# Kernel optimization log

Measured on AMD Instinct MI355X. Metric: run time of the kernel, lower is better.

The kernel has to match this reference:

```python
import jax, jax.numpy as jnp
import numpy as np

H = W = 512
P = H * W          # total superpixel member pixels
N_SP = 1024        # number of superpixels


def _conv(x, w, b):
    # x: [N,C,H,W], w: [O,I,3,3] -> [N,O,H,W], SAME padding
    y = jax.lax.conv_general_dilated(
        x, w, window_strides=(1, 1), padding='SAME',
        dimension_numbers=('NCHW', 'OIHW', 'NCHW'))
    return y + b[None, :, None, None]


def _embed(raw, w1, b1, w2, b2, w3, b3):
    h = jax.nn.relu(_conv(raw, w1, b1))
    h = jax.nn.relu(_conv(h, w2, b2))
    return _conv(h, w3, b3)  # [1, 10, H, W]


def setup_inputs() -> dict:
    key = jax.random.key(0)
    ks = jax.random.split(key, 6)
    raw = jax.random.normal(ks[0], (1, 1, H, W), dtype=jnp.float32)
    w1 = jax.random.normal(ks[1], (64, 1, 3, 3), dtype=jnp.float32) * 0.3
    b1 = jnp.zeros((64,), jnp.float32)
    w2 = jax.random.normal(ks[2], (64, 64, 3, 3), dtype=jnp.float32) * 0.05
    b2 = jnp.zeros((64,), jnp.float32)
    w3 = jax.random.normal(ks[3], (10, 64, 3, 3), dtype=jnp.float32) * 0.05
    b3 = jnp.zeros((10,), jnp.float32)
    pix_rc = jax.random.randint(ks[4], (P, 2), 0, H, dtype=jnp.int32)
    seg_ids = jax.random.randint(ks[5], (P,), 0, N_SP, dtype=jnp.int32)
    return {"raw": raw, "w1": w1, "b1": b1, "w2": w2, "b2": b2,
            "w3": w3, "b3": b3, "pix_rc": pix_rc, "seg_ids": seg_ids,
            "n_sp": N_SP}


def reference(raw, w1, b1, w2, b2, w3, b3, pix_rc, seg_ids, n_sp):
    feats = _embed(raw, w1, b1, w2, b2, w3, b3)  # [1, C, H, W]
    f = feats[0]                                  # [C, H, W]
    # gather per-pixel feature vectors: [P, C]
    vals = f[:, pix_rc[:, 0], pix_rc[:, 1]].T
    # scatter-mean over superpixels (= per-sp sum / mass)
    sums = jax.ops.segment_sum(vals, seg_ids, num_segments=n_sp)      # [n_sp, C]
    cnts = jax.ops.segment_sum(jnp.ones((vals.shape[0],), vals.dtype),
                               seg_ids, num_segments=n_sp)            # [n_sp]
    return sums / jnp.maximum(cnts, 1.0)[:, None]
```

## Files before the change

### kernel.cpp

```cpp
#include <hip/hip_runtime.h>

typedef __attribute__((ext_vector_type(8))) short short8;
typedef __attribute__((ext_vector_type(4))) float f32x4;

constexpr int H = 512, W = 512;
constexpr int P = H * W;
constexpr int NSP = 1024;
constexpr int SBLK = 512;
constexpr int FGRP = 16;

__device__ inline unsigned short f2bf(float f) {
  unsigned u = __builtin_bit_cast(unsigned, f);
  unsigned r = (u + 0x7fffu + ((u >> 16) & 1u)) >> 16;
  return (unsigned short)r;
}
__device__ inline float bflo(unsigned u) { return __builtin_bit_cast(float, u << 16); }
__device__ inline float bfhi(unsigned u) { return __builtin_bit_cast(float, u & 0xffff0000u); }

__device__ inline int xcd_swz(int b, int cpx) { return (b & 7) * cpx + (b >> 3); }

__global__ __launch_bounds__(256) void prep_k(const float* __restrict__ w2,
                                              const float* __restrict__ w3,
                                              unsigned short* __restrict__ wt2s,
                                              unsigned short* __restrict__ wt3s,
                                              unsigned short* __restrict__ zeros) {
  if (blockIdx.x == 0 && threadIdx.x < 128) zeros[threadIdx.x] = 0;
  int i = blockIdx.x * 256 + threadIdx.x;
  if (i < 36864) {
    int k = i >> 11;
    int t = (i >> 3) & 255;
    int e = i & 7;
    int r = t >> 2, sp = t & 3, s = sp ^ (r & 3);
    int tap = k >> 1, ic = (k & 1) * 32 + s * 8 + e;
    wt2s[i] = f2bf(w2[r * 576 + ic * 9 + tap]);
  } else if (i < 46080) {
    int j = i - 36864;
    int k = j >> 9;
    int t = (j >> 3) & 63;
    int e = j & 7;
    int r = t >> 2, sp = t & 3, s = sp ^ (r & 3);
    int tap = k >> 1, ic = (k & 1) * 32 + s * 8 + e;
    wt3s[j] = (r < 10) ? f2bf(w3[r * 576 + ic * 9 + tap]) : (unsigned short)0;
  }
}

__device__ inline void stage_acts(const unsigned short* __restrict__ xin,
                                  const unsigned short* __restrict__ zeros,
                                  unsigned short* acts, int r0, int c0,
                                  int wave, int lane) {
  for (int wi = wave; wi < 26; wi += 4) {
    int cidx = wi * 64 + lane;
    int pix = cidx >> 3, slotp = cidx & 7;
    int prow = pix / 34, pcol = pix - prow * 34;
    int gr = r0 + prow - 1, gc = c0 + pcol - 1;
    int slot = slotp ^ (pix & 7);
    bool ok = (pix < 204) & ((unsigned)gr < 512u) & ((unsigned)gc < 512u);
    const unsigned short* src = ok ? (xin + (((size_t)(gr * 512 + gc)) << 6) + slot * 8) : zeros;
    unsigned short* dstb = &acts[wi * 512];
    __builtin_amdgcn_global_load_lds((const __attribute__((address_space(1))) void*)src,
                                     (__attribute__((address_space(3))) void*)dstb, 16, 0, 0);
  }
}

__global__ __launch_bounds__(256) void conv2_k(const float* __restrict__ raw,
                                               const float* __restrict__ w1,
                                               const float* __restrict__ b1,
                                               const unsigned short* __restrict__ wts,
                                               const float* __restrict__ bias,
                                               unsigned short* __restrict__ ynhwc) {
  constexpr int WCS = 2048;
  __shared__ __align__(16) unsigned short acts[208 * 64];
  __shared__ __align__(16) unsigned short wbuf[3 * WCS];
  __shared__ float rawt[9 * 36];
  int tid = threadIdx.x;
  int lane = tid & 63, wave = tid >> 6;
  int logical = xcd_swz(blockIdx.x, 256);
  int tilex = logical & 15, tiley = logical >> 4;
  int c0 = tilex * 32, r0 = tiley * 4;

#pragma unroll
  for (int k0 = 0; k0 < 2; ++k0) {
    const unsigned short* src = wts + (size_t)k0 * WCS + tid * 8;
    unsigned short* dstb = wbuf + k0 * WCS + wave * 512;
    __builtin_amdgcn_global_load_lds((const __attribute__((address_space(1))) void*)src,
                                     (__attribute__((address_space(3))) void*)dstb, 16, 0, 0);
  }
  for (int i = tid; i < 324; i += 256) {
    int rr = i / 36, cc = i - rr * 36;
    int gr = r0 + rr - 2, gc = c0 + cc - 2;
    bool ok = ((unsigned)gr < 512u) && ((unsigned)gc < 512u);
    rawt[i] = ok ? raw[gr * 512 + gc] : 0.f;
  }

  int q = lane >> 4, n = lane & 15;
  short8 a1f;
  {
    short av[8];
#pragma unroll
    for (int e = 0; e < 8; ++e) av[e] = 0;
    int oc = wave * 16 + n;
    if (q == 0) {
#pragma unroll
      for (int e = 0; e < 8; ++e) av[e] = (short)f2bf(w1[oc * 9 + e]);
    } else if (q == 1) {
      av[0] = (short)f2bf(w1[oc * 9 + 8]);
    }
    a1f = (short8){av[0], av[1], av[2], av[3], av[4], av[5], av[6], av[7]};
  }
  float bb1[4];
#pragma unroll
  for (int r2 = 0; r2 < 4; ++r2) bb1[r2] = b1[wave * 16 + q * 4 + r2];
  __syncthreads();

  char* actw = (char*)acts;
  for (int t = 0; t < 13; ++t) {
    int px = t * 16 + n;
    int prow = px / 34, pcol = px - prow * 34;
    short bv[8];
#pragma unroll
    for (int e = 0; e < 8; ++e) bv[e] = 0;
    if (q == 0) {
#pragma unroll
      for (int e = 0; e < 8; ++e) {
        int dy = e / 3, dx = e - dy * 3;
        bv[e] = (short)f2bf(rawt[(prow + dy) * 36 + pcol + dx]);
      }
    } else if (q == 1) {
      bv[0] = (short)f2bf(rawt[(prow + 2) * 36 + pcol + 2]);
    }
    short8 b1f = (short8){bv[0], bv[1], bv[2], bv[3], bv[4], bv[5], bv[6], bv[7]};
    f32x4 d = __builtin_amdgcn_mfma_f32_16x16x32_bf16(a1f, b1f,
                                                       (f32x4){0.f, 0.f, 0.f, 0.f}, 0, 0, 0);
    int gr1 = r0 + prow - 1, gc1 = c0 + pcol - 1;
    bool ok1 = ((unsigned)gr1 < 512u) && ((unsigned)gc1 < 512u);
    float o0 = ok1 ? fmaxf(d.x + bb1[0], 0.f) : 0.f;
    float o1 = ok1 ? fmaxf(d.y + bb1[1], 0.f) : 0.f;
    float o2 = ok1 ? fmaxf(d.z + bb1[2], 0.f) : 0.f;
    float o3 = ok1 ? fmaxf(d.w + bb1[3], 0.f) : 0.f;
    unsigned lo = (unsigned)f2bf(o0) | ((unsigned)f2bf(o1) << 16);
    unsigned hi = (unsigned)f2bf(o2) | ((unsigned)f2bf(o3) << 16);
    int wa = px * 128 + ((((wave * 2 + (q >> 1)) ^ (px & 7)) << 4)) + ((q & 1) << 3);
    *reinterpret_cast<uint2*>(actw + wa) = make_uint2(lo, hi);
  }
  __syncthreads();

  f32x4 acc[4][2];
#pragma unroll
  for (int og = 0; og < 4; ++og)
#pragma unroll
    for (int g = 0; g < 2; ++g) acc[og][g] = (f32x4){0.f, 0.f, 0.f, 0.f};

  int plbase[2];
#pragma unroll
  for (int g = 0; g < 2; ++g) plbase[g] = wave * 34 + 16 * g + n;
  const char* actb = (const char*)acts;

#pragma unroll
  for (int k = 0; k < 18; ++k) {
    if (k == 17) {
      asm volatile("s_waitcnt vmcnt(0)" ::: "memory");
    } else {
      asm volatile("s_waitcnt vmcnt(1)" ::: "memory");
    }
    __builtin_amdgcn_sched_barrier(0);
    __builtin_amdgcn_s_barrier();
    __builtin_amdgcn_sched_barrier(0);
    if (k + 2 < 18) {
      const unsigned short* src = wts + (size_t)(k + 2) * WCS + tid * 8;
      unsigned short* dstb = wbuf + ((k + 2) % 3) * WCS + wave * 512;
      __builtin_amdgcn_global_load_lds((const __attribute__((address_space(1))) void*)src,
                                       (__attribute__((address_space(3))) void*)dstb, 16, 0, 0);
    }
    const int tap = k >> 1, kc = k & 1;
    const int kyy = tap / 3, kxx = tap - kyy * 3;
    const char* wb = (const char*)(wbuf + (k % 3) * WCS);
    short8 af[4];
#pragma unroll
    for (int og = 0; og < 4; ++og) {
      int r = og * 16 + n;
      af[og] = *reinterpret_cast<const short8*>(wb + r * 64 + ((q ^ (r & 3)) * 16));
    }
#pragma unroll
    for (int g = 0; g < 2; ++g) {
      int pl = plbase[g] + kyy * 34 + kxx;
      int addr = pl * 128 + (((kc * 4 + q) ^ (pl & 7)) * 16);
      short8 bf = *reinterpret_cast<const short8*>(actb + addr);
#pragma unroll
      for (int og = 0; og < 4; ++og)
        acc[og][g] = __builtin_amdgcn_mfma_f32_16x16x32_bf16(af[og], bf, acc[og][g], 0, 0, 0);
    }
  }

  __syncthreads();
  char* ob = (char*)acts;
#pragma unroll
  for (int og = 0; og < 4; ++og) {
    float b0 = bias[og * 16 + q * 4 + 0], b1v = bias[og * 16 + q * 4 + 1];
    float b2 = bias[og * 16 + q * 4 + 2], b3 = bias[og * 16 + q * 4 + 3];
#pragma unroll
    for (int g = 0; g < 2; ++g) {
      int pl = wave * 32 + g * 16 + n;
      f32x4 v = acc[og][g];
      float o0 = fmaxf(v.x + b0, 0.f), o1 = fmaxf(v.y + b1v, 0.f);
      float o2 = fmaxf(v.z + b2, 0.f), o3 = fmaxf(v.w + b3, 0.f);
      unsigned lo = (unsigned)f2bf(o0) | ((unsigned)f2bf(o1) << 16);
      unsigned hi = (unsigned)f2bf(o2) | ((unsigned)f2bf(o3) << 16);
      int lslot = og * 2 + (q >> 1);
      int wa = pl * 128 + (((lslot ^ (pl & 7)) << 4)) + ((q & 1) << 3);
      *reinterpret_cast<uint2*>(ob + wa) = make_uint2(lo, hi);
    }
  }
  __syncthreads();
  char* yb = (char*)ynhwc;
#pragma unroll
  for (int it = 0; it < 4; ++it) {
    int c = it * 256 + tid;
    int pl = c >> 3, slot = c & 7;
    uint4 v = *reinterpret_cast<const uint4*>(ob + pl * 128 + ((slot ^ (pl & 7)) << 4));
    size_t gb = (((size_t)(r0 + (pl >> 5)) * 512) + c0 + (pl & 31)) * 128 + slot * 16;
    *reinterpret_cast<uint4*>(yb + gb) = v;
  }
}

__global__ __launch_bounds__(256) void conv3_k(const unsigned short* __restrict__ xin,
                                               const unsigned short* __restrict__ wts,
                                               const float* __restrict__ bias,
                                               unsigned short* __restrict__ feats,
                                               const unsigned short* __restrict__ zeros) {
  __shared__ __align__(16) unsigned short acts[208 * 64];
  __shared__ __align__(16) unsigned short wl[9216];
  int tid = threadIdx.x;
  int lane = tid & 63, wave = tid >> 6;
  int logical = xcd_swz(blockIdx.x, 256);
  int tilex = logical & 15, tiley = logical >> 4;
  int c0 = tilex * 32, r0 = tiley * 4;

  stage_acts(xin, zeros, acts, r0, c0, wave, lane);
  for (int wi = wave; wi < 18; wi += 4) {
    const unsigned short* src = wts + (size_t)wi * 512 + lane * 8;
    unsigned short* dstb = &wl[wi * 512];
    __builtin_amdgcn_global_load_lds((const __attribute__((address_space(1))) void*)src,
                                     (__attribute__((address_space(3))) void*)dstb, 16, 0, 0);
  }
  __syncthreads();

  int q = lane >> 4, n = lane & 15;
  f32x4 acc[2];
#pragma unroll
  for (int g = 0; g < 2; ++g) acc[g] = (f32x4){0.f, 0.f, 0.f, 0.f};
  int plbase[2];
#pragma unroll
  for (int g = 0; g < 2; ++g) plbase[g] = wave * 34 + 16 * g + n;
  const char* actb = (const char*)acts;
  const char* wb0 = (const char*)wl;

#pragma unroll
  for (int k = 0; k < 18; ++k) {
    const int tap = k >> 1, kc = k & 1;
    const int kyy = tap / 3, kxx = tap - kyy * 3;
    short8 af = *reinterpret_cast<const short8*>(wb0 + k * 1024 + n * 64 + ((q ^ (n & 3)) * 16));
#pragma unroll
    for (int g = 0; g < 2; ++g) {
      int pl = plbase[g] + kyy * 34 + kxx;
      int addr = pl * 128 + (((kc * 4 + q) ^ (pl & 7)) * 16);
      short8 bf = *reinterpret_cast<const short8*>(actb + addr);
      acc[g] = __builtin_amdgcn_mfma_f32_16x16x32_bf16(af, bf, acc[g], 0, 0, 0);
    }
  }

  __syncthreads();
  char* ob = (char*)acts;
  float bb[4];
#pragma unroll
  for (int r2 = 0; r2 < 4; ++r2) {
    int oc = q * 4 + r2;
    bb[r2] = (oc < 10) ? bias[oc] : 0.f;
  }
#pragma unroll
  for (int g = 0; g < 2; ++g) {
    int pl = wave * 32 + g * 16 + n;
    f32x4 v = acc[g];
    float o0 = v.x + bb[0], o1 = v.y + bb[1], o2 = v.z + bb[2], o3 = v.w + bb[3];
    if (q < 2) {
      unsigned u0 = (unsigned)f2bf(o0) | ((unsigned)f2bf(o1) << 16);
      unsigned u1 = (unsigned)f2bf(o2) | ((unsigned)f2bf(o3) << 16);
      *reinterpret_cast<uint2*>(ob + pl * 24 + q * 8) = make_uint2(u0, u1);
    } else if (q == 2) {
      *reinterpret_cast<unsigned*>(ob + pl * 24 + 16) =
          (unsigned)f2bf(o0) | ((unsigned)f2bf(o1) << 16);
    }
  }
  __syncthreads();
  char* fb = (char*)feats;
  {
    int c = tid;
    for (int it = 0; it < 3 && c < 640; ++it, c += 256) {
      int row = c / 160, wb = c - row * 160;
      int byte = wb * 4;
      int px = byte / 20, off = byte - px * 20;
      unsigned v = *reinterpret_cast<const unsigned*>(ob + (row * 32 + px) * 24 + off);
      size_t gbyte = (((size_t)(r0 + row) * 512) + c0) * 20 + (size_t)byte;
      *reinterpret_cast<unsigned*>(fb + gbyte) = v;
    }
  }
}

__global__ __launch_bounds__(256) void scatter_k(const unsigned short* __restrict__ feats,
                                                 const int* __restrict__ pix_rc,
                                                 const int* __restrict__ seg,
                                                 float* __restrict__ partials) {
  __shared__ float ls[NSP * 10];
  __shared__ float lc[NSP];
  int tid = threadIdx.x;
  for (int i = tid; i < NSP * 10; i += 256) ls[i] = 0.f;
  for (int i = tid; i < NSP; i += 256) lc[i] = 0.f;
  __syncthreads();

  constexpr int PER = P / SBLK;
  int p0 = blockIdx.x * PER;
  for (int p = p0 + tid; p < p0 + PER; p += 256) {
    int r = pix_rc[2 * p], c = pix_rc[2 * p + 1];
    int s = seg[p];
    size_t gpix = (size_t)r * 512 + c;
    const char* fp = (const char*)feats + gpix * 20;
    uint4 a = *reinterpret_cast<const uint4*>(fp);
    unsigned e = *reinterpret_cast<const unsigned*>(fp + 16);
    float v[10];
    v[0] = bflo(a.x); v[1] = bfhi(a.x);
    v[2] = bflo(a.y); v[3] = bfhi(a.y);
    v[4] = bflo(a.z); v[5] = bfhi(a.z);
    v[6] = bflo(a.w); v[7] = bfhi(a.w);
    v[8] = bflo(e);   v[9] = bfhi(e);
#pragma unroll
    for (int ch = 0; ch < 10; ++ch) atomicAdd(&ls[s * 10 + ch], v[ch]);
    atomicAdd(&lc[s], 1.f);
  }
  __syncthreads();

  float* outp = partials + (size_t)blockIdx.x * (NSP * 11);
  for (int i = tid; i < NSP * 10; i += 256) outp[i] = ls[i];
  for (int i = tid; i < NSP; i += 256) outp[NSP * 10 + i] = lc[i];
}

__global__ __launch_bounds__(256) void finA_k(const float* __restrict__ partials,
                                              float* __restrict__ partials2) {
  int g = blockIdx.x / 44;
  int e = (blockIdx.x - g * 44) * 256 + threadIdx.x;
  const float* base = partials + (size_t)(g * 32) * (NSP * 11) + e;
  float s = 0.f;
#pragma unroll 8
  for (int k = 0; k < 32; ++k) s += base[(size_t)k * (NSP * 11)];
  partials2[(size_t)g * (NSP * 11) + e] = s;
}

__global__ __launch_bounds__(256) void finB_k(const float* __restrict__ partials2,
                                              float* __restrict__ out) {
  int i = blockIdx.x * 256 + threadIdx.x;
  if (i >= NSP * 10) return;
  int sp = i / 10;
  float s = 0.f, cnt = 0.f;
#pragma unroll
  for (int g = 0; g < FGRP; ++g) {
    const float* pp = partials2 + (size_t)g * (NSP * 11);
    s += pp[i];
    cnt += pp[NSP * 10 + sp];
  }
  out[i] = s / fmaxf(cnt, 1.f);
}

extern "C" void kernel_launch(void* const* d_in, const int* in_sizes, int n_in,
                              void* d_out, int out_size, void* d_ws, size_t ws_size,
                              hipStream_t stream) {
  const float* raw = (const float*)d_in[0];
  const float* w1  = (const float*)d_in[1];
  const float* b1  = (const float*)d_in[2];
  const float* w2  = (const float*)d_in[3];
  const float* b2  = (const float*)d_in[4];
  const float* w3  = (const float*)d_in[5];
  const float* b3  = (const float*)d_in[6];
  const int* pix_rc = (const int*)d_in[7];
  const int* seg    = (const int*)d_in[8];
  float* out = (float*)d_out;

  char* ws = (char*)d_ws;
  unsigned short* h2   = (unsigned short*)(ws + 33554432);
  unsigned short* feats = (unsigned short*)(ws + 67108864);
  unsigned short* wt2s = (unsigned short*)(ws + 72351744);
  unsigned short* wt3s = (unsigned short*)(ws + 72425472);
  unsigned short* zeros = (unsigned short*)(ws + 72443904);
  float* partials  = (float*)(ws + 0);
  float* partials2 = (float*)(ws + 23068672);

  prep_k<<<180, 256, 0, stream>>>(w2, w3, wt2s, wt3s, zeros);
  conv2_k<<<2048, 256, 0, stream>>>(raw, w1, b1, wt2s, b2, h2);
  conv3_k<<<2048, 256, 0, stream>>>(h2, wt3s, b3, feats, zeros);
  scatter_k<<<SBLK, 256, 0, stream>>>(feats, pix_rc, seg, partials);
  finA_k<<<FGRP * 44, 256, 0, stream>>>(partials, partials2);
  finB_k<<<40, 256, 0, stream>>>(partials2, out);
}
```

Measured before the change: 84.62 us.

## Double conv tile height to 8 rows with 512-thread blocks

Conv2 and conv3 tiles grow from 4x32 to 8x32 pixels, with 512 threads per block and half as many blocks. This lowers the halo overhead per tile (10 rows staged for 8 output rows instead of 6 for 4) and spreads each weight load over twice the outputs. Conv1 recompute in conv2 is split across the two wave halves, and scatter_k also moves to 512 threads. The cost is more LDS per block and fewer blocks, which may reduce occupancy and latency hiding.

```diff
diff --git a/kernel.cpp b/kernel.cpp
--- a/kernel.cpp
+++ b/kernel.cpp
@@ -44,61 +44,46 @@
   }
 }
 
-__device__ inline void stage_acts(const unsigned short* __restrict__ xin,
-                                  const unsigned short* __restrict__ zeros,
-                                  unsigned short* acts, int r0, int c0,
-                                  int wave, int lane) {
-  for (int wi = wave; wi < 26; wi += 4) {
-    int cidx = wi * 64 + lane;
-    int pix = cidx >> 3, slotp = cidx & 7;
-    int prow = pix / 34, pcol = pix - prow * 34;
-    int gr = r0 + prow - 1, gc = c0 + pcol - 1;
-    int slot = slotp ^ (pix & 7);
-    bool ok = (pix < 204) & ((unsigned)gr < 512u) & ((unsigned)gc < 512u);
-    const unsigned short* src = ok ? (xin + (((size_t)(gr * 512 + gc)) << 6) + slot * 8) : zeros;
-    unsigned short* dstb = &acts[wi * 512];
-    __builtin_amdgcn_global_load_lds((const __attribute__((address_space(1))) void*)src,
-                                     (__attribute__((address_space(3))) void*)dstb, 16, 0, 0);
-  }
-}
-
-__global__ __launch_bounds__(256) void conv2_k(const float* __restrict__ raw,
+__global__ __launch_bounds__(512) void conv2_k(const float* __restrict__ raw,
                                                const float* __restrict__ w1,
                                                const float* __restrict__ b1,
                                                const unsigned short* __restrict__ wts,
                                                const float* __restrict__ bias,
                                                unsigned short* __restrict__ ynhwc) {
   constexpr int WCS = 2048;
-  __shared__ __align__(16) unsigned short acts[208 * 64];
+  __shared__ __align__(16) unsigned short acts[352 * 64];
   __shared__ __align__(16) unsigned short wbuf[3 * WCS];
-  __shared__ float rawt[9 * 36];
+  __shared__ float rawt[12 * 36];
   int tid = threadIdx.x;
   int lane = tid & 63, wave = tid >> 6;
-  int logical = xcd_swz(blockIdx.x, 256);
+  int logical = xcd_swz(blockIdx.x, 128);
   int tilex = logical & 15, tiley = logical >> 4;
-  int c0 = tilex * 32, r0 = tiley * 4;
-
-#pragma unroll
-  for (int k0 = 0; k0 < 2; ++k0) {
-    const unsigned short* src = wts + (size_t)k0 * WCS + tid * 8;
-    unsigned short* dstb = wbuf + k0 * WCS + wave * 512;
-    __builtin_amdgcn_global_load_lds((const __attribute__((address_space(1))) void*)src,
-                                     (__attribute__((address_space(3))) void*)dstb, 16, 0, 0);
-  }
-  for (int i = tid; i < 324; i += 256) {
-    int rr = i / 36, cc = i - rr * 36;
+  int c0 = tilex * 32, r0 = tiley * 8;
+
+  if (tid < 256) {
+#pragma unroll
+    for (int k0 = 0; k0 < 2; ++k0) {
+      const unsigned short* src = wts + (size_t)k0 * WCS + tid * 8;
+      unsigned short* dstb = wbuf + k0 * WCS + wave * 512;
+      __builtin_amdgcn_global_load_lds((const __attribute__((address_space(1))) void*)src,
+                                       (__attribute__((address_space(3))) void*)dstb, 16, 0, 0);
+    }
+  }
+  if (tid < 432) {
+    int rr = tid / 36, cc = tid - rr * 36;
     int gr = r0 + rr - 2, gc = c0 + cc - 2;
     bool ok = ((unsigned)gr < 512u) && ((unsigned)gc < 512u);
-    rawt[i] = ok ? raw[gr * 512 + gc] : 0.f;
+    rawt[tid] = ok ? raw[gr * 512 + gc] : 0.f;
   }
 
   int q = lane >> 4, n = lane & 15;
+  int og1 = wave & 3;
   short8 a1f;
   {
     short av[8];
 #pragma unroll
     for (int e = 0; e < 8; ++e) av[e] = 0;
-    int oc = wave * 16 + n;
+    int oc = og1 * 16 + n;
     if (q == 0) {
 #pragma unroll
       for (int e = 0; e < 8; ++e) av[e] = (short)f2bf(w1[oc * 9 + e]);
@@ -109,13 +94,17 @@
   }
   float bb1[4];
 #pragma unroll
-  for (int r2 = 0; r2 < 4; ++r2) bb1[r2] = b1[wave * 16 + q * 4 + r2];
+  for (int r2 = 0; r2 < 4; ++r2) bb1[r2] = b1[og1 * 16 + q * 4 + r2];
   __syncthreads();
 
   char* actw = (char*)acts;
-  for (int t = 0; t < 13; ++t) {
+  int tbase = (wave < 4) ? 0 : 11;
+  for (int ti = 0; ti < 11; ++ti) {
+    int t = tbase + ti;
     int px = t * 16 + n;
+    bool okp = px < 340;
     int prow = px / 34, pcol = px - prow * 34;
+    int prc = okp ? prow : 9;
     short bv[8];
 #pragma unroll
     for (int e = 0; e < 8; ++e) bv[e] = 0;
@@ -123,23 +112,23 @@
 #pragma unroll
       for (int e = 0; e < 8; ++e) {
         int dy = e / 3, dx = e - dy * 3;
-        bv[e] = (short)f2bf(rawt[(prow + dy) * 36 + pcol + dx]);
+        bv[e] = (short)f2bf(rawt[(prc + dy) * 36 + pcol + dx]);
       }
     } else if (q == 1) {
-      bv[0] = (short)f2bf(rawt[(prow + 2) * 36 + pcol + 2]);
+      bv[0] = (short)f2bf(rawt[(prc + 2) * 36 + pcol + 2]);
     }
     short8 b1f = (short8){bv[0], bv[1], bv[2], bv[3], bv[4], bv[5], bv[6], bv[7]};
     f32x4 d = __builtin_amdgcn_mfma_f32_16x16x32_bf16(a1f, b1f,
                                                        (f32x4){0.f, 0.f, 0.f, 0.f}, 0, 0, 0);
     int gr1 = r0 + prow - 1, gc1 = c0 + pcol - 1;
-    bool ok1 = ((unsigned)gr1 < 512u) && ((unsigned)gc1 < 512u);
+    bool ok1 = okp && ((unsigned)gr1 < 512u) && ((unsigned)gc1 < 512u);
     float o0 = ok1 ? fmaxf(d.x + bb1[0], 0.f) : 0.f;
     float o1 = ok1 ? fmaxf(d.y + bb1[1], 0.f) : 0.f;
     float o2 = ok1 ? fmaxf(d.z + bb1[2], 0.f) : 0.f;
     float o3 = ok1 ? fmaxf(d.w + bb1[3], 0.f) : 0.f;
     unsigned lo = (unsigned)f2bf(o0) | ((unsigned)f2bf(o1) << 16);
     unsigned hi = (unsigned)f2bf(o2) | ((unsigned)f2bf(o3) << 16);
-    int wa = px * 128 + ((((wave * 2 + (q >> 1)) ^ (px & 7)) << 4)) + ((q & 1) << 3);
+    int wa = px * 128 + ((((og1 * 2 + (q >> 1)) ^ (px & 7)) << 4)) + ((q & 1) << 3);
     *reinterpret_cast<uint2*>(actw + wa) = make_uint2(lo, hi);
   }
   __syncthreads();
@@ -165,7 +154,7 @@
     __builtin_amdgcn_sched_barrier(0);
     __builtin_amdgcn_s_barrier();
     __builtin_amdgcn_sched_barrier(0);
-    if (k + 2 < 18) {
+    if (k + 2 < 18 && tid < 256) {
       const unsigned short* src = wts + (size_t)(k + 2) * WCS + tid * 8;
       unsigned short* dstb = wbuf + ((k + 2) % 3) * WCS + wave * 512;
       __builtin_amdgcn_global_load_lds((const __attribute__((address_space(1))) void*)src,
@@ -214,7 +203,7 @@
   char* yb = (char*)ynhwc;
 #pragma unroll
   for (int it = 0; it < 4; ++it) {
-    int c = it * 256 + tid;
+    int c = it * 512 + tid;
     int pl = c >> 3, slot = c & 7;
     uint4 v = *reinterpret_cast<const uint4*>(ob + pl * 128 + ((slot ^ (pl & 7)) << 4));
     size_t gb = (((size_t)(r0 + (pl >> 5)) * 512) + c0 + (pl & 31)) * 128 + slot * 16;
@@ -222,23 +211,34 @@
   }
 }
 
-__global__ __launch_bounds__(256) void conv3_k(const unsigned short* __restrict__ xin,
+__global__ __launch_bounds__(512) void conv3_k(const unsigned short* __restrict__ xin,
                                                const unsigned short* __restrict__ wts,
                                                const float* __restrict__ bias,
                                                unsigned short* __restrict__ feats,
                                                const unsigned short* __restrict__ zeros) {
-  __shared__ __align__(16) unsigned short acts[208 * 64];
+  __shared__ __align__(16) unsigned short acts[352 * 64];
   __shared__ __align__(16) unsigned short wl[9216];
   int tid = threadIdx.x;
   int lane = tid & 63, wave = tid >> 6;
-  int logical = xcd_swz(blockIdx.x, 256);
+  int logical = xcd_swz(blockIdx.x, 128);
   int tilex = logical & 15, tiley = logical >> 4;
-  int c0 = tilex * 32, r0 = tiley * 4;
-
-  stage_acts(xin, zeros, acts, r0, c0, wave, lane);
-  for (int wi = wave; wi < 18; wi += 4) {
+  int c0 = tilex * 32, r0 = tiley * 8;
+
+  for (int wi = wave; wi < 18; wi += 8) {
     const unsigned short* src = wts + (size_t)wi * 512 + lane * 8;
     unsigned short* dstb = &wl[wi * 512];
+    __builtin_amdgcn_global_load_lds((const __attribute__((address_space(1))) void*)src,
+                                     (__attribute__((address_space(3))) void*)dstb, 16, 0, 0);
+  }
+  for (int wi = wave; wi < 44; wi += 8) {
+    int cidx = wi * 64 + lane;
+    int pix = cidx >> 3, slotp = cidx & 7;
+    int prow = pix / 34, pcol = pix - prow * 34;
+    int gr = r0 + prow - 1, gc = c0 + pcol - 1;
+    int slot = slotp ^ (pix & 7);
+    bool ok = (pix < 340) & ((unsigned)gr < 512u) & ((unsigned)gc < 512u);
+    const unsigned short* src = ok ? (xin + (((size_t)(gr * 512 + gc)) << 6) + slot * 8) : zeros;
+    unsigned short* dstb = &acts[wi * 512];
     __builtin_amdgcn_global_load_lds((const __attribute__((address_space(1))) void*)src,
                                      (__attribute__((address_space(3))) void*)dstb, 16, 0, 0);
   }
@@ -292,9 +292,10 @@
   }
   __syncthreads();
   char* fb = (char*)feats;
-  {
-    int c = tid;
-    for (int it = 0; it < 3 && c < 640; ++it, c += 256) {
+#pragma unroll
+  for (int it = 0; it < 3; ++it) {
+    int c = it * 512 + tid;
+    if (c < 1280) {
       int row = c / 160, wb = c - row * 160;
       int byte = wb * 4;
       int px = byte / 20, off = byte - px * 20;
@@ -305,20 +306,20 @@
   }
 }
 
-__global__ __launch_bounds__(256) void scatter_k(const unsigned short* __restrict__ feats,
+__global__ __launch_bounds__(512) void scatter_k(const unsigned short* __restrict__ feats,
                                                  const int* __restrict__ pix_rc,
                                                  const int* __restrict__ seg,
                                                  float* __restrict__ partials) {
   __shared__ float ls[NSP * 10];
   __shared__ float lc[NSP];
   int tid = threadIdx.x;
-  for (int i = tid; i < NSP * 10; i += 256) ls[i] = 0.f;
-  for (int i = tid; i < NSP; i += 256) lc[i] = 0.f;
+  for (int i = tid; i < NSP * 10; i += 512) ls[i] = 0.f;
+  for (int i = tid; i < NSP; i += 512) lc[i] = 0.f;
   __syncthreads();
 
   constexpr int PER = P / SBLK;
   int p0 = blockIdx.x * PER;
-  for (int p = p0 + tid; p < p0 + PER; p += 256) {
+  for (int p = p0 + tid; p < p0 + PER; p += 512) {
     int r = pix_rc[2 * p], c = pix_rc[2 * p + 1];
     int s = seg[p];
     size_t gpix = (size_t)r * 512 + c;
@@ -338,8 +339,8 @@
   __syncthreads();
 
   float* outp = partials + (size_t)blockIdx.x * (NSP * 11);
-  for (int i = tid; i < NSP * 10; i += 256) outp[i] = ls[i];
-  for (int i = tid; i < NSP; i += 256) outp[NSP * 10 + i] = lc[i];
+  for (int i = tid; i < NSP * 10; i += 512) outp[i] = ls[i];
+  for (int i = tid; i < NSP; i += 512) outp[NSP * 10 + i] = lc[i];
 }
 
 __global__ __launch_bounds__(256) void finA_k(const float* __restrict__ partials,
@@ -392,9 +393,9 @@
   float* partials2 = (float*)(ws + 23068672);
 
   prep_k<<<180, 256, 0, stream>>>(w2, w3, wt2s, wt3s, zeros);
-  conv2_k<<<2048, 256, 0, stream>>>(raw, w1, b1, wt2s, b2, h2);
-  conv3_k<<<2048, 256, 0, stream>>>(h2, wt3s, b3, feats, zeros);
-  scatter_k<<<SBLK, 256, 0, stream>>>(feats, pix_rc, seg, partials);
+  conv2_k<<<1024, 512, 0, stream>>>(raw, w1, b1, wt2s, b2, h2);
+  conv3_k<<<1024, 512, 0, stream>>>(h2, wt3s, b3, feats, zeros);
+  scatter_k<<<SBLK, 512, 0, stream>>>(feats, pix_rc, seg, partials);
   finA_k<<<FGRP * 44, 256, 0, stream>>>(partials, partials2);
   finB_k<<<40, 256, 0, stream>>>(partials2, out);
 }
```

Measured after the change: 83.66 us. No clear change (-1.1%).
